# Optimization experiments

Hardware: AMD Instinct MI355X
Metric: run time of the kernel (lower is better)

Reference implementation:

```python
import jax, jax.numpy as jnp
import numpy as np

ALPHA = 0.1
EPS = 1e-7

def proj(x):
    # Re-project onto hyperboloid: time coord t = sqrt(1 + |s|^2)
    s = x[:, 1:]
    t = jnp.sqrt(1.0 + jnp.sum(s * s, axis=-1, keepdims=True))
    return jnp.concatenate([t, s], axis=-1)

def linner(x, y):
    # Lorentzian inner product <x,y>_L = -x0*y0 + <xs, ys>
    return -x[..., 0] * y[..., 0] + jnp.sum(x[..., 1:] * y[..., 1:], axis=-1)

def safe_acosh(z):
    return jnp.arccosh(jnp.maximum(z, 1.0 + EPS))

def setup_inputs() -> dict:
    key = jax.random.key(0)
    k1, k2 = jax.random.split(key)
    B, n, A = 1_000_000, 64, 16
    s = jax.random.normal(k1, (B, n), dtype=jnp.float32) * 0.5
    t = jnp.sqrt(1.0 + jnp.sum(s * s, axis=-1, keepdims=True))
    hyp_emb = jnp.concatenate([t, s], axis=-1)  # [B, n+1] on hyperboloid
    a_s = jax.random.normal(k2, (A, n), dtype=jnp.float32) * 0.01
    a_t = jnp.sqrt(1.0 + jnp.sum(a_s * a_s, axis=-1, keepdims=True))
    anchors = jnp.concatenate([a_t, a_s], axis=-1)  # [A, n+1]
    return {"hyp_emb": hyp_emb, "anchors": anchors}

def reference(hyp_emb, anchors):
    anchors_p = proj(anchors)  # [A, d]
    # Lorentzian pairwise inner products [B, A]
    inner = (-hyp_emb[:, :1] * anchors_p[None, :, 0]
             + jnp.einsum('bd,ad->ba', hyp_emb[:, 1:], anchors_p[:, 1:]))
    dists = safe_acosh(-inner)
    nearest_idx = jnp.argmin(dists, axis=1)        # [B]
    na = anchors_p[nearest_idx]                    # [B, d] gather
    # log_map_x(y): d(x,y) * (y + <x,y> x) / ||y + <x,y> x||_L
    xy = linner(hyp_emb, na)                       # [B]
    d = safe_acosh(-xy)
    u = na + xy[:, None] * hyp_emb
    unorm = jnp.sqrt(jnp.maximum(linner(u, u), EPS))
    v = (ALPHA * d / unorm)[:, None] * u           # alpha * direction
    # exp_map_x(v): cosh(|v|) x + sinh(|v|) v / |v|
    vn = jnp.sqrt(jnp.maximum(linner(v, v), EPS * EPS))
    sinhc = jnp.where(vn > EPS, jnp.sinh(vn) / vn, 1.0)
    out = jnp.cosh(vn)[:, None] * hyp_emb + sinhc[:, None] * v
    return out
```

## Files before the change

### kernel.cpp

```cpp
#include <hip/hip_runtime.h>
#include <math.h>

#define ALPHA 0.1f
#define EPS 1e-7f

constexpr int D = 65;
constexpr int A = 16;
constexpr int ROWS = 256;

__global__ void prep_anchors(const float* __restrict__ anchors,
                             float* __restrict__ ws) {
    __shared__ float s_a[A * D];
    int tid = threadIdx.x;
    for (int i = tid; i < A * D; i += blockDim.x) s_a[i] = anchors[i];
    __syncthreads();
    if (tid < A) {
        float s = 0.f;
        for (int j = 1; j < D; ++j) {
            float v = s_a[tid * D + j];
            s = fmaf(v, v, s);
        }
        s_a[tid * D] = sqrtf(1.f + s);
    }
    __syncthreads();
    for (int i = tid; i < A * D; i += blockDim.x) {
        int a = i / D, j = i % D;
        ws[j * A + a]  = s_a[i];
        ws[A * D + i]  = s_a[i];
    }
}

__global__ __launch_bounds__(ROWS) void
homeo_kernel(const float* __restrict__ x,
             const float* __restrict__ aT,
             const float* __restrict__ aRM,
             float* __restrict__ out, int B) {
    __shared__ float xs[ROWS * D];
    __shared__ float anch[A * D];

    const int tid = threadIdx.x;
    const long rowStart = (long)blockIdx.x * ROWS;
    const int nRows = min(ROWS, B - (int)rowStart);
    const int nF4 = nRows * D / 4;

    const float4* g4 = (const float4*)(x + rowStart * D);
    float4* s4 = (float4*)xs;
    for (int i = tid; i < nF4; i += ROWS) s4[i] = g4[i];
    for (int i = tid; i < A * D; i += ROWS) anch[i] = aRM[i];
    __syncthreads();

    if (tid < nRows) {
        float xr[D];
#pragma unroll
        for (int j = 0; j < D; ++j) xr[j] = xs[tid * D + j];

        float acc[A];
#pragma unroll
        for (int a = 0; a < A; ++a) acc[a] = -xr[0] * aT[a];
#pragma unroll
        for (int j = 1; j < D; ++j) {
            const float xj = xr[j];
#pragma unroll
            for (int a = 0; a < A; ++a)
                acc[a] = fmaf(xj, aT[j * A + a], acc[a]);
        }

        const float onePlusEps = 1.0f + EPS;
        float bestZ = fmaxf(-acc[0], onePlusEps);
        float xy = acc[0];
        int bidx = 0;
#pragma unroll
        for (int a = 1; a < A; ++a) {
            float z = fmaxf(-acc[a], onePlusEps);
            if (z < bestZ) { bestZ = z; bidx = a; xy = acc[a]; }
        }

        const float d = acoshf(bestZ);
        const float* na = anch + bidx * D;

        float uu;
        {
            float u0 = fmaf(xy, xr[0], na[0]);
            uu = -u0 * u0;
#pragma unroll
            for (int j = 1; j < D; ++j) {
                float uj = fmaf(xy, xr[j], na[j]);
                uu = fmaf(uj, uj, uu);
            }
        }
        const float unorm = sqrtf(fmaxf(uu, EPS));
        const float c = ALPHA * d / unorm;
        const float vv = c * c * uu;
        const float vn = sqrtf(fmaxf(vv, EPS * EPS));
        const float sinhc = (vn > EPS) ? (sinhf(vn) / vn) : 1.0f;
        const float ch = coshf(vn);
        const float sc = sinhc * c;

#pragma unroll
        for (int j = 0; j < D; ++j) {
            float uj = fmaf(xy, xr[j], na[j]);
            xs[tid * D + j] = fmaf(ch, xr[j], sc * uj);
        }
    }
    __syncthreads();

    float4* o4 = (float4*)(out + rowStart * D);
    for (int i = tid; i < nF4; i += ROWS) o4[i] = s4[i];
}

extern "C" void kernel_launch(void* const* d_in, const int* in_sizes, int n_in,
                              void* d_out, int out_size, void* d_ws, size_t ws_size,
                              hipStream_t stream) {
    const float* hyp = (const float*)d_in[0];
    const float* anchors = (const float*)d_in[1];
    float* out = (float*)d_out;
    float* ws = (float*)d_ws;

    const int B = in_sizes[0] / D;

    prep_anchors<<<1, 256, 0, stream>>>(anchors, ws);

    const int grid = (B + ROWS - 1) / ROWS;
    homeo_kernel<<<grid, ROWS, 0, stream>>>(hyp, ws, ws + A * D, out, B);
}
```

Before: 485.7 us.

## Per-wave async global-to-LDS row staging and drop block-wide sync before store

Each wave now owns 64 rows and loads its slice directly into LDS with global_load_lds async copies instead of register-staged float4 copies. The block-wide barrier before the output copy is replaced by a per-wave LDS wait, so waves can write back independently. The chosen anchor row is also copied into registers before use, and launch bounds request two blocks per CU. Possible risks: ordering of the async LDS writes relative to the single __syncthreads, and higher register pressure from the extra 65-float array.

```diff
diff --git a/kernel.cpp b/kernel.cpp
--- a/kernel.cpp
+++ b/kernel.cpp
@@ -1,12 +1,29 @@
 #include <hip/hip_runtime.h>
 #include <math.h>
+#include <stdint.h>
 
 #define ALPHA 0.1f
 #define EPS 1e-7f
 
 constexpr int D = 65;
 constexpr int A = 16;
-constexpr int ROWS = 256;
+constexpr int WPB = 4;
+constexpr int TPB = WPB * 64;
+constexpr int RPW = 64;
+constexpr int WAVE_FLOATS = RPW * D;
+
+__device__ __forceinline__ void async_cp16(const float* g, float* l) {
+    __builtin_amdgcn_global_load_lds(
+        (const __attribute__((address_space(1))) uint32_t*)(uintptr_t)g,
+        (__attribute__((address_space(3))) uint32_t*)(uint32_t)(uintptr_t)l,
+        16, 0, 0);
+}
+__device__ __forceinline__ void async_cp4(const float* g, float* l) {
+    __builtin_amdgcn_global_load_lds(
+        (const __attribute__((address_space(1))) uint32_t*)(uintptr_t)g,
+        (__attribute__((address_space(3))) uint32_t*)(uint32_t)(uintptr_t)l,
+        4, 0, 0);
+}
 
 __global__ void prep_anchors(const float* __restrict__ anchors,
                              float* __restrict__ ws) {
@@ -25,34 +42,47 @@
     __syncthreads();
     for (int i = tid; i < A * D; i += blockDim.x) {
         int a = i / D, j = i % D;
-        ws[j * A + a]  = s_a[i];
-        ws[A * D + i]  = s_a[i];
+        ws[j * A + a] = s_a[i];
+        ws[A * D + i] = s_a[i];
     }
 }
 
-__global__ __launch_bounds__(ROWS) void
+__global__ __launch_bounds__(TPB, 2) void
 homeo_kernel(const float* __restrict__ x,
              const float* __restrict__ aT,
              const float* __restrict__ aRM,
-             float* __restrict__ out, int B) {
-    __shared__ float xs[ROWS * D];
+             float* __restrict__ out, int B, int nWG) {
+    __shared__ float xs[WPB * WAVE_FLOATS];
     __shared__ float anch[A * D];
 
     const int tid = threadIdx.x;
-    const long rowStart = (long)blockIdx.x * ROWS;
-    const int nRows = min(ROWS, B - (int)rowStart);
-    const int nF4 = nRows * D / 4;
+    const int wave = tid >> 6;
+    const int lane = tid & 63;
+    const int wg = blockIdx.x * WPB + wave;
+    const bool active = wg < nWG;
 
-    const float4* g4 = (const float4*)(x + rowStart * D);
-    float4* s4 = (float4*)xs;
-    for (int i = tid; i < nF4; i += ROWS) s4[i] = g4[i];
-    for (int i = tid; i < A * D; i += ROWS) anch[i] = aRM[i];
+    float* lbase = xs + wave * WAVE_FLOATS;
+    const long rowStart = (long)wg * RPW;
+    const int nRows = active ? (int)min((long)RPW, (long)B - rowStart) : 0;
+
+    if (active && nRows == RPW) {
+        const float* gbase = x + rowStart * D;
+#pragma unroll
+        for (int c = 0; c < 16; ++c)
+            async_cp16(gbase + c * 256 + lane * 4, lbase + c * 256);
+        async_cp4(gbase + 16 * 256 + lane, lbase + 16 * 256);
+    } else if (active && lane < nRows) {
+        for (int j = 0; j < D; ++j)
+            lbase[lane * D + j] = x[(rowStart + lane) * D + j];
+    }
+
+    for (int i = tid; i < A * D; i += TPB) anch[i] = aRM[i];
     __syncthreads();
 
-    if (tid < nRows) {
+    if (active && lane < nRows) {
         float xr[D];
 #pragma unroll
-        for (int j = 0; j < D; ++j) xr[j] = xs[tid * D + j];
+        for (int j = 0; j < D; ++j) xr[j] = lbase[lane * D + j];
 
         float acc[A];
 #pragma unroll
@@ -74,19 +104,21 @@
             float z = fmaxf(-acc[a], onePlusEps);
             if (z < bestZ) { bestZ = z; bidx = a; xy = acc[a]; }
         }
+        const float d = acoshf(bestZ);
 
-        const float d = acoshf(bestZ);
-        const float* na = anch + bidx * D;
+        float nar[D];
+#pragma unroll
+        for (int j = 0; j < D; ++j) nar[j] = anch[bidx * D + j];
 
         float uu;
         {
-            float u0 = fmaf(xy, xr[0], na[0]);
+            float u0 = fmaf(xy, xr[0], nar[0]);
             uu = -u0 * u0;
+        }
 #pragma unroll
-            for (int j = 1; j < D; ++j) {
-                float uj = fmaf(xy, xr[j], na[j]);
-                uu = fmaf(uj, uj, uu);
-            }
+        for (int j = 1; j < D; ++j) {
+            float uj = fmaf(xy, xr[j], nar[j]);
+            uu = fmaf(uj, uj, uu);
         }
         const float unorm = sqrtf(fmaxf(uu, EPS));
         const float c = ALPHA * d / unorm;
@@ -98,14 +130,23 @@
 
 #pragma unroll
         for (int j = 0; j < D; ++j) {
-            float uj = fmaf(xy, xr[j], na[j]);
-            xs[tid * D + j] = fmaf(ch, xr[j], sc * uj);
+            float uj = fmaf(xy, xr[j], nar[j]);
+            lbase[lane * D + j] = fmaf(ch, xr[j], sc * uj);
         }
     }
-    __syncthreads();
 
-    float4* o4 = (float4*)(out + rowStart * D);
-    for (int i = tid; i < nF4; i += ROWS) o4[i] = s4[i];
+    asm volatile("s_waitcnt lgkmcnt(0)" ::: "memory");
+
+    if (active && nRows == RPW) {
+        float4* o4 = (float4*)(out + rowStart * D);
+        const float4* l4 = (const float4*)lbase;
+#pragma unroll
+        for (int c = 0; c < 16; ++c) o4[c * 64 + lane] = l4[c * 64 + lane];
+        out[rowStart * D + 16 * 256 + lane] = lbase[16 * 256 + lane];
+    } else if (active && lane < nRows) {
+        for (int j = 0; j < D; ++j)
+            out[(rowStart + lane) * D + j] = lbase[lane * D + j];
+    }
 }
 
 extern "C" void kernel_launch(void* const* d_in, const int* in_sizes, int n_in,
@@ -117,9 +158,9 @@
     float* ws = (float*)d_ws;
 
     const int B = in_sizes[0] / D;
+    const int nWG = (B + RPW - 1) / RPW;
+    const int grid = (nWG + WPB - 1) / WPB;
 
     prep_anchors<<<1, 256, 0, stream>>>(anchors, ws);
-
-    const int grid = (B + ROWS - 1) / ROWS;
-    homeo_kernel<<<grid, ROWS, 0, stream>>>(hyp, ws, ws + A * D, out, B);
+    homeo_kernel<<<grid, TPB, 0, stream>>>(hyp, ws, ws + A * D, out, B, nWG);
 }
```

New measurement: 441.0 us. 9.2% less time.
